# Kernel tuning notes

Measured on AMD Instinct MI355X. Metric: run time of the kernel, lower is better.

## Reference

```python
import jax, jax.numpy as jnp
import numpy as np

H, F, E_SHARED, E_ROUTED, K = 1024, 4096, 1, 8, 2


def setup_inputs() -> dict:
    key = jax.random.key(0)
    ks = jax.random.split(key, 6)
    x = jax.random.normal(ks[0], (4, 2048, H), dtype=jnp.float32)
    s = 0.02
    shared_up = jax.random.normal(ks[1], (E_SHARED, H, F), dtype=jnp.float32) * s
    shared_down = jax.random.normal(ks[2], (E_SHARED, F, H), dtype=jnp.float32) * s
    routed_up = jax.random.normal(ks[3], (E_ROUTED, H, F), dtype=jnp.float32) * s
    routed_down = jax.random.normal(ks[4], (E_ROUTED, F, H), dtype=jnp.float32) * s
    router_w = jax.random.normal(ks[5], (H, E_ROUTED), dtype=jnp.float32) * s
    return {"x": x, "shared_up": shared_up, "shared_down": shared_down,
            "routed_up": routed_up, "routed_down": routed_down, "router_w": router_w}


def _expert(x, w_up, w_down):
    # ExpertBlock: down(gelu(up(x))), exact (erf) gelu as in torch F.gelu default
    h = jax.nn.gelu(jnp.einsum('bsh,hf->bsf', x, w_up), approximate=False)
    return jnp.einsum('bsf,fh->bsh', h, w_down)


def reference(x, shared_up, shared_down, routed_up, routed_down, router_w):
    # shared experts (always active)
    shared_out = jnp.zeros_like(x)
    for i in range(E_SHARED):
        shared_out = shared_out + _expert(x, shared_up[i], shared_down[i])

    # router: softmax over routed experts, then top-k gating
    probs = jax.nn.softmax(jnp.einsum('bsh,he->bse', x, router_w), axis=-1)
    top_k_prob, top_k_idx = jax.lax.top_k(probs, K)  # [B,S,K]
    # per-expert gate = sum of top-k probs assigned to that expert
    onehot = jax.nn.one_hot(top_k_idx, E_ROUTED, dtype=x.dtype)  # [B,S,K,E]
    gates = jnp.einsum('bsk,bske->bse', top_k_prob, onehot)      # [B,S,E]

    routed_out = jnp.zeros_like(x)
    for e in range(E_ROUTED):  # fixed small loop over experts
        y = _expert(x, routed_up[e], routed_down[e])
        routed_out = routed_out + gates[..., e:e + 1] * y

    return shared_out + routed_out + x
```

## Files before the change

### kernel.cpp

```cpp
#include <hip/hip_runtime.h>
#include <cstdint>
#include <cstddef>

#define HD 1024
#define FF 4096
#define TOK 8192
#define NSEG 9
#define ROWS_ROUTED (TOK*2)
#define ROWS_TOT (ROWS_ROUTED + TOK)

typedef __bf16 bf16;
typedef __bf16 bf16x8 __attribute__((ext_vector_type(8)));
typedef __bf16 bf16x4 __attribute__((ext_vector_type(4)));
typedef float  f32x4  __attribute__((ext_vector_type(4)));

__device__ __forceinline__ void stage16(const void* g, void* l) {
  __builtin_amdgcn_global_load_lds((const __attribute__((address_space(1))) void*)g,
                                   (__attribute__((address_space(3))) void*)l,
                                   16, 0, 0);
}

__device__ __forceinline__ unsigned short bf_bits(float v) {
  bf16 b = (bf16)v;
  return __builtin_bit_cast(unsigned short, b);
}

__device__ __forceinline__ int xcd_remap(int d) {
  return (((d >> 6) << 3) + (d & 7)) * 8 + ((d >> 3) & 7);
}

__global__ void k_init_meta(int* meta) {
  int t = threadIdx.x;
  if (t < 64) meta[t] = 0;
}

__global__ void k_tcvt(const float* __restrict__ routed_up, const float* __restrict__ shared_up,
                       const float* __restrict__ routed_dn, const float* __restrict__ shared_dn,
                       bf16* __restrict__ wupT, bf16* __restrict__ wdnT) {
  int z = blockIdx.z;
  bool isup = z < 9;
  int e = isup ? z : z - 9;
  const float* src = isup ? ((e < 8) ? (routed_up + (size_t)e*HD*FF) : shared_up)
                          : ((e < 8) ? (routed_dn + (size_t)e*FF*HD) : shared_dn);
  bf16* d = (isup ? wupT : wdnT) + (size_t)e*FF*HD;
  int R = isup ? HD : FF, C = isup ? FF : HD;
  int r0 = (isup ? blockIdx.y : blockIdx.x) * 64;
  int c0 = (isup ? blockIdx.x : blockIdx.y) * 64;
  __shared__ float lds[64][65];
  int t = threadIdx.x;
  int tr = t>>4, tc4 = (t&15)*4;
  #pragma unroll
  for (int i=0;i<4;i++) {
    float4 v = *reinterpret_cast<const float4*>(src + (size_t)(r0+tr+i*16)*C + c0 + tc4);
    lds[tr+i*16][tc4+0]=v.x; lds[tr+i*16][tc4+1]=v.y;
    lds[tr+i*16][tc4+2]=v.z; lds[tr+i*16][tc4+3]=v.w;
  }
  __syncthreads();
  #pragma unroll
  for (int i=0;i<4;i++) {
    int oc = tr + i*16;
    ushort4 u;
    u.x = bf_bits(lds[tc4+0][oc]);
    u.y = bf_bits(lds[tc4+1][oc]);
    u.z = bf_bits(lds[tc4+2][oc]);
    u.w = bf_bits(lds[tc4+3][oc]);
    *reinterpret_cast<ushort4*>(d + (size_t)(c0+oc)*R + r0 + tc4) = u;
  }
}

__global__ void k_router(const float* __restrict__ x, const float* __restrict__ rw,
                         bf16* __restrict__ xbf,
                         int* __restrict__ rtE, float* __restrict__ rtG,
                         int* __restrict__ meta) {
  __shared__ float rwl[HD*8];
  int t = threadIdx.x;
  for (int i=t;i<HD*8/4;i+=256)
    reinterpret_cast<float4*>(rwl)[i] = reinterpret_cast<const float4*>(rw)[i];
  __syncthreads();
  int wv = t>>6, lane = t&63;
  int tk = blockIdx.x*4 + wv;
  const float* xr = x + (size_t)tk*HD;
  bf16* xb = xbf + (size_t)tk*HD;
  float a[8] = {0,0,0,0,0,0,0,0};
  for (int i=0;i<HD/64;i++) {
    int h = lane + i*64;
    float xv = xr[h];
    xb[h] = (bf16)xv;
    const float* r = rwl + h*8;
    #pragma unroll
    for (int e=0;e<8;e++) a[e] = fmaf(xv, r[e], a[e]);
  }
  #pragma unroll
  for (int e=0;e<8;e++) {
    for (int s=32;s>0;s>>=1) a[e] += __shfl_xor(a[e], s, 64);
  }
  if (lane==0) {
    float mx = a[0];
    #pragma unroll
    for (int e=1;e<8;e++) mx = fmaxf(mx, a[e]);
    float p[8]; float den = 0.f;
    #pragma unroll
    for (int e=0;e<8;e++) { p[e] = expf(a[e]-mx); den += p[e]; }
    int i0 = 0;
    #pragma unroll
    for (int e=1;e<8;e++) if (p[e] > p[i0]) i0 = e;
    int i1 = (i0==0)?1:0;
    #pragma unroll
    for (int e=0;e<8;e++) if (e!=i0 && p[e] > p[i1]) i1 = e;
    float inv = 1.f/den;
    rtE[tk*2] = i0; rtE[tk*2+1] = i1;
    rtG[tk*2] = p[i0]*inv; rtG[tk*2+1] = p[i1]*inv;
    atomicAdd(&meta[i0], 1);
    atomicAdd(&meta[i1], 1);
  }
}

__global__ void k_prefix(int* meta) {
  if (threadIdx.x == 0) {
    int off = 0;
    for (int e=0;e<8;e++) { meta[16+e] = off; meta[32+e] = meta[e]; off += meta[e]; }
    meta[16+8] = ROWS_ROUTED;
    meta[32+8] = TOK;
  }
}

__global__ void k_scatter(const int* __restrict__ rtE, const float* __restrict__ rtG,
                          int* __restrict__ meta, int* __restrict__ tok,
                          float* __restrict__ gate, int* __restrict__ trow) {
  int t = blockIdx.x*256 + threadIdx.x;
  int e0 = rtE[t*2], e1 = rtE[t*2+1];
  float g0 = rtG[t*2], g1 = rtG[t*2+1];
  int p0 = atomicAdd(&meta[8+e0], 1);
  int r0 = meta[16+e0] + p0;
  tok[r0] = t; gate[r0] = g0; trow[t*2] = r0;
  int p1 = atomicAdd(&meta[8+e1], 1);
  int r1 = meta[16+e1] + p1;
  tok[r1] = t; gate[r1] = g1; trow[t*2+1] = r1;
  tok[ROWS_ROUTED + t] = t; gate[ROWS_ROUTED + t] = 1.0f;
}

__global__ void k_combine(const float* __restrict__ x, const bf16* __restrict__ dbuf,
                          const int* __restrict__ trow, float* __restrict__ out) {
  int tkn = blockIdx.x;
  int t = threadIdx.x;
  int r0 = trow[tkn*2], r1 = trow[tkn*2+1];
  int h = t*4;
  float4 xv = *reinterpret_cast<const float4*>(x + (size_t)tkn*HD + h);
  bf16x4 a = *reinterpret_cast<const bf16x4*>(dbuf + (size_t)(ROWS_ROUTED+tkn)*HD + h);
  bf16x4 b = *reinterpret_cast<const bf16x4*>(dbuf + (size_t)r0*HD + h);
  bf16x4 c = *reinterpret_cast<const bf16x4*>(dbuf + (size_t)r1*HD + h);
  float4 o;
  o.x = xv.x + (float)a[0] + (float)b[0] + (float)c[0];
  o.y = xv.y + (float)a[1] + (float)b[1] + (float)c[1];
  o.z = xv.z + (float)a[2] + (float)b[2] + (float)c[2];
  o.w = xv.w + (float)a[3] + (float)b[3] + (float)c[3];
  *reinterpret_cast<float4*>(out + (size_t)tkn*HD + h) = o;
}


#define BUFSZ 24576
#define NKU (HD/32)
#define NKD (FF/32)

__global__ __launch_bounds__(512,4) void k_gemm_up(
    const bf16* __restrict__ xbf, const bf16* __restrict__ wupT,
    bf16* __restrict__ hbuf, const int* __restrict__ tok,
    const int* __restrict__ meta)
{
  int bx = xcd_remap(blockIdx.x);
  int seg = bx >> 10;
  int rem = bx & 1023;
  int mt = rem >> 5, nt = rem & 31;
  int rows = (seg<8)? meta[32+seg] : TOK;
  if (mt*256 >= rows) return;
  int segoff = meta[16+seg];
  int rowbase = mt*256;

  __shared__ __align__(16) char lds[3*BUFSZ];

  const int t = threadIdx.x;
  const int lane = t & 63, w = t >> 6;
  const int wm = w >> 1, wn = w & 1;

  int ar = t>>2;
  int kswz = ((t&3) ^ ((t>>3)&3)) * 8;
  int gr0 = rowbase + ar;        if (gr0 >= rows) gr0 = rows-1;
  int gr1 = rowbase + 128 + ar;  if (gr1 >= rows) gr1 = rows-1;
  const bf16* gA0 = xbf + (size_t)tok[segoff+gr0]*HD + kswz;
  const bf16* gA1 = xbf + (size_t)tok[segoff+gr1]*HD + kswz;
  const bf16* wb = wupT + (size_t)seg*FF*HD;
  const bf16* gB = wb + (size_t)(nt*128 + ar)*HD + kswz;
  const int dA0 = t*16, dA1 = 8192 + t*16, dB = 16384 + t*16;

  const int sx = ((lane>>4) ^ (((lane&15)>>1)&3)) * 16;
  const int Afo = (wm*64 + (lane&15))*64 + sx;
  const int Bfo = 16384 + (wn*64 + (lane&15))*64 + sx;

  f32x4 acc[4][4] = {};

  stage16(gA0,    lds + dA0); stage16(gA1,    lds + dA1); stage16(gB,    lds + dB);
  stage16(gA0+32, lds + BUFSZ + dA0); stage16(gA1+32, lds + BUFSZ + dA1);
  stage16(gB+32,  lds + BUFSZ + dB);
  asm volatile("s_waitcnt vmcnt(3)" ::: "memory");
  __builtin_amdgcn_s_barrier();

  int cur = 0;
  for (int kt = 0; kt < NKU; ++kt) {
    if (kt + 2 < NKU) {
      int st = (cur >= 1) ? cur - 1 : 2;
      int ko = (kt+2)*32;
      char* nb = lds + st*BUFSZ;
      stage16(gA0+ko, nb + dA0); stage16(gA1+ko, nb + dA1); stage16(gB+ko, nb + dB);
    }
    const char* cb = lds + cur*BUFSZ;
    bf16x8 af[4], bfr[4];
    #pragma unroll
    for (int m=0;m<4;m++) af[m]  = *reinterpret_cast<const bf16x8*>(cb + Afo + m*1024);
    #pragma unroll
    for (int n=0;n<4;n++) bfr[n] = *reinterpret_cast<const bf16x8*>(cb + Bfo + n*1024);
    #pragma unroll
    for (int m=0;m<4;m++)
      #pragma unroll
      for (int n=0;n<4;n++)
        acc[m][n] = __builtin_amdgcn_mfma_f32_16x16x32_bf16(bfr[n], af[m], acc[m][n], 0,0,0);
    if (kt + 2 < NKU)      asm volatile("s_waitcnt vmcnt(3)" ::: "memory");
    else if (kt + 1 < NKU) asm volatile("s_waitcnt vmcnt(0)" ::: "memory");
    if (kt + 1 < NKU) __builtin_amdgcn_s_barrier();
    cur = (cur >= 2) ? 0 : cur + 1;
  }

  const int lrm = lane&15, lq = lane>>4;
  #pragma unroll
  for (int m=0;m<4;m++) {
    int rl = wm*64 + m*16 + lrm;
    int gr = rowbase + rl;
    if (gr >= rows) continue;
    bf16* hrow = hbuf + (size_t)(segoff+gr)*FF + nt*128 + wn*64 + lq*4;
    #pragma unroll
    for (int n=0;n<4;n++) {
      bf16x4 u;
      #pragma unroll
      for (int j=0;j<4;j++) {
        float v = acc[m][n][j];
        v = 0.5f*v*(1.0f + erff(v*0.70710678118654752f));
        u[j] = (bf16)v;
      }
      *reinterpret_cast<bf16x4*>(hrow + n*16) = u;
    }
  }
}

__global__ __launch_bounds__(512,4) void k_gemm_down(
    const bf16* __restrict__ hbuf, const bf16* __restrict__ wdnT,
    bf16* __restrict__ dbuf, const float* __restrict__ gate,
    const int* __restrict__ meta)
{
  int bx = xcd_remap(blockIdx.x);
  int seg = bx >> 8;
  int rem = bx & 255;
  int mt = rem >> 3, nt = rem & 7;
  int rows = (seg<8)? meta[32+seg] : TOK;
  if (mt*256 >= rows) return;
  int segoff = meta[16+seg];
  int rowbase = mt*256;

  __shared__ __align__(16) char lds[3*BUFSZ];
  __shared__ float gateL[256];

  const int t = threadIdx.x;
  const int lane = t & 63, w = t >> 6;
  const int wm = w >> 1, wn = w & 1;

  if (t < 256) {
    int gr = rowbase + t; if (gr >= rows) gr = rows - 1;
    gateL[t] = gate[segoff + gr];
  }

  int ar = t>>2;
  int kswz = ((t&3) ^ ((t>>3)&3)) * 8;
  const bf16* gA0 = hbuf + (size_t)(segoff + rowbase + ar)*FF + kswz;
  const bf16* gA1 = hbuf + (size_t)(segoff + rowbase + 128 + ar)*FF + kswz;
  const bf16* wb = wdnT + (size_t)seg*HD*FF;
  const bf16* gB = wb + (size_t)(nt*128 + ar)*FF + kswz;
  const int dA0 = t*16, dA1 = 8192 + t*16, dB = 16384 + t*16;

  const int sx = ((lane>>4) ^ (((lane&15)>>1)&3)) * 16;
  const int Afo = (wm*64 + (lane&15))*64 + sx;
  const int Bfo = 16384 + (wn*64 + (lane&15))*64 + sx;

  f32x4 acc[4][4] = {};

  stage16(gA0,    lds + dA0); stage16(gA1,    lds + dA1); stage16(gB,    lds + dB);
  stage16(gA0+32, lds + BUFSZ + dA0); stage16(gA1+32, lds + BUFSZ + dA1);
  stage16(gB+32,  lds + BUFSZ + dB);
  asm volatile("s_waitcnt vmcnt(3)" ::: "memory");
  __builtin_amdgcn_s_barrier();

  int cur = 0;
  for (int kt = 0; kt < NKD; ++kt) {
    if (kt + 2 < NKD) {
      int st = (cur >= 1) ? cur - 1 : 2;
      int ko = (kt+2)*32;
      char* nb = lds + st*BUFSZ;
      stage16(gA0+ko, nb + dA0); stage16(gA1+ko, nb + dA1); stage16(gB+ko, nb + dB);
    }
    const char* cb = lds + cur*BUFSZ;
    bf16x8 af[4], bfr[4];
    #pragma unroll
    for (int m=0;m<4;m++) af[m]  = *reinterpret_cast<const bf16x8*>(cb + Afo + m*1024);
    #pragma unroll
    for (int n=0;n<4;n++) bfr[n] = *reinterpret_cast<const bf16x8*>(cb + Bfo + n*1024);
    #pragma unroll
    for (int m=0;m<4;m++)
      #pragma unroll
      for (int n=0;n<4;n++)
        acc[m][n] = __builtin_amdgcn_mfma_f32_16x16x32_bf16(bfr[n], af[m], acc[m][n], 0,0,0);
    if (kt + 2 < NKD)      asm volatile("s_waitcnt vmcnt(3)" ::: "memory");
    else if (kt + 1 < NKD) asm volatile("s_waitcnt vmcnt(0)" ::: "memory");
    if (kt + 1 < NKD) __builtin_amdgcn_s_barrier();
    cur = (cur >= 2) ? 0 : cur + 1;
  }

  const int lrm = lane&15, lq = lane>>4;
  #pragma unroll
  for (int m=0;m<4;m++) {
    int rl = wm*64 + m*16 + lrm;
    int gr = rowbase + rl;
    if (gr >= rows) continue;
    float g = gateL[rl];
    bf16* drow = dbuf + (size_t)(segoff+gr)*HD + nt*128 + wn*64 + lq*4;
    #pragma unroll
    for (int n=0;n<4;n++) {
      bf16x4 u;
      #pragma unroll
      for (int j=0;j<4;j++) u[j] = (bf16)(acc[m][n][j]*g);
      *reinterpret_cast<bf16x4*>(drow + n*16) = u;
    }
  }
}

struct Layout {
  size_t xbf, wupT, wdnT, hbuf, dbuf, tok, gate, trow, rtE, rtG, meta, total;
};

static inline Layout make_layout() {
  Layout L; size_t o = 0;
  auto al = [&](size_t b){ o = (o+255)&~(size_t)255; size_t r=o; o+=b; return r; };
  L.xbf  = al((size_t)TOK*HD*2);
  L.wupT = al((size_t)NSEG*FF*HD*2);
  L.wdnT = al((size_t)NSEG*FF*HD*2);
  L.hbuf = al((size_t)ROWS_TOT*FF*2);
  L.dbuf = al((size_t)ROWS_TOT*HD*2);
  L.tok  = al((size_t)ROWS_TOT*4);
  L.gate = al((size_t)ROWS_TOT*4);
  L.trow = al((size_t)TOK*2*4);
  L.rtE  = al((size_t)TOK*2*4);
  L.rtG  = al((size_t)TOK*2*4);
  L.meta = al(256*4);
  L.total = o;
  return L;
}

extern "C" void kernel_launch(void* const* d_in, const int* in_sizes, int n_in,
                              void* d_out, int out_size, void* d_ws, size_t ws_size,
                              hipStream_t stream) {
  const float* x           = (const float*)d_in[0];
  const float* shared_up   = (const float*)d_in[1];
  const float* shared_down = (const float*)d_in[2];
  const float* routed_up   = (const float*)d_in[3];
  const float* routed_down = (const float*)d_in[4];
  const float* router_w    = (const float*)d_in[5];
  float* out = (float*)d_out;

  Layout L = make_layout();
  char* ws = (char*)d_ws;
  bf16*  xbf  = (bf16*)(ws + L.xbf);
  bf16*  wupT = (bf16*)(ws + L.wupT);
  bf16*  wdnT = (bf16*)(ws + L.wdnT);
  bf16*  hbuf = (bf16*)(ws + L.hbuf);
  bf16*  dbuf = (bf16*)(ws + L.dbuf);
  int*   tok  = (int*)(ws + L.tok);
  float* gate = (float*)(ws + L.gate);
  int*   trow = (int*)(ws + L.trow);
  int*   rtE  = (int*)(ws + L.rtE);
  float* rtG  = (float*)(ws + L.rtG);
  int*   meta = (int*)(ws + L.meta);

  k_init_meta<<<1, 64, 0, stream>>>(meta);
  k_tcvt<<<dim3(64, 16, 18), 256, 0, stream>>>(routed_up, shared_up, routed_down, shared_down, wupT, wdnT);
  k_router<<<TOK/4, 256, 0, stream>>>(x, router_w, xbf, rtE, rtG, meta);
  k_prefix<<<1, 64, 0, stream>>>(meta);
  k_scatter<<<TOK/256, 256, 0, stream>>>(rtE, rtG, meta, tok, gate, trow);

  k_gemm_up<<<NSEG*32*32, 512, 0, stream>>>(xbf, wupT, hbuf, tok, meta);
  k_gemm_down<<<NSEG*32*8, 512, 0, stream>>>(hbuf, wdnT, dbuf, gate, meta);
  k_combine<<<TOK, 256, 0, stream>>>(x, dbuf, trow, out);
}
```

Baseline: 988.8 us.

## Fold meta init and prefix into other kernels; double-buffer down GEMM

New measurement: 2.078 ms. +110.2%, slower.

```diff
diff --git a/kernel.cpp b/kernel.cpp
--- a/kernel.cpp
+++ b/kernel.cpp
@@ -29,14 +29,13 @@
   return (((d >> 6) << 3) + (d & 7)) * 8 + ((d >> 3) & 7);
 }
 
-__global__ void k_init_meta(int* meta) {
-  int t = threadIdx.x;
-  if (t < 64) meta[t] = 0;
-}
 
 __global__ void k_tcvt(const float* __restrict__ routed_up, const float* __restrict__ shared_up,
                        const float* __restrict__ routed_dn, const float* __restrict__ shared_dn,
-                       bf16* __restrict__ wupT, bf16* __restrict__ wdnT) {
+                       bf16* __restrict__ wupT, bf16* __restrict__ wdnT,
+                       int* __restrict__ meta) {
+  if (blockIdx.z == 0 && blockIdx.x == 0 && blockIdx.y == 0 && threadIdx.x < 64)
+    meta[threadIdx.x] = 0;
   int z = blockIdx.z;
   bool isup = z < 9;
   int e = isup ? z : z - 9;
@@ -115,28 +114,34 @@
   }
 }
 
-__global__ void k_prefix(int* meta) {
-  if (threadIdx.x == 0) {
-    int off = 0;
-    for (int e=0;e<8;e++) { meta[16+e] = off; meta[32+e] = meta[e]; off += meta[e]; }
-    meta[16+8] = ROWS_ROUTED;
-    meta[32+8] = TOK;
-  }
-}
-
 __global__ void k_scatter(const int* __restrict__ rtE, const float* __restrict__ rtG,
                           int* __restrict__ meta, int* __restrict__ tok,
                           float* __restrict__ gate, int* __restrict__ trow) {
-  int t = blockIdx.x*256 + threadIdx.x;
-  int e0 = rtE[t*2], e1 = rtE[t*2+1];
-  float g0 = rtG[t*2], g1 = rtG[t*2+1];
+  __shared__ int soff[8];
+  int t = threadIdx.x;
+  if (t == 0) {
+    int off = 0;
+    #pragma unroll
+    for (int e=0;e<8;e++) { soff[e] = off; off += meta[e]; }
+    if (blockIdx.x == 0) {
+      int o2 = 0;
+      #pragma unroll
+      for (int e=0;e<8;e++) { meta[16+e] = o2; meta[32+e] = meta[e]; o2 += meta[e]; }
+      meta[16+8] = ROWS_ROUTED;
+      meta[32+8] = TOK;
+    }
+  }
+  __syncthreads();
+  int tk = blockIdx.x*256 + t;
+  int e0 = rtE[tk*2], e1 = rtE[tk*2+1];
+  float g0 = rtG[tk*2], g1 = rtG[tk*2+1];
   int p0 = atomicAdd(&meta[8+e0], 1);
-  int r0 = meta[16+e0] + p0;
-  tok[r0] = t; gate[r0] = g0; trow[t*2] = r0;
+  int r0 = soff[e0] + p0;
+  tok[r0] = tk; gate[r0] = g0; trow[tk*2] = r0;
   int p1 = atomicAdd(&meta[8+e1], 1);
-  int r1 = meta[16+e1] + p1;
-  tok[r1] = t; gate[r1] = g1; trow[t*2+1] = r1;
-  tok[ROWS_ROUTED + t] = t; gate[ROWS_ROUTED + t] = 1.0f;
+  int r1 = soff[e1] + p1;
+  tok[r1] = tk; gate[r1] = g1; trow[tk*2+1] = r1;
+  tok[ROWS_ROUTED + tk] = tk; gate[ROWS_ROUTED + tk] = 1.0f;
 }
 
 __global__ void k_combine(const float* __restrict__ x, const bf16* __restrict__ dbuf,
@@ -250,7 +255,8 @@
   }
 }
 
-__global__ __launch_bounds__(512,4) void k_gemm_down(
+
+__global__ __launch_bounds__(512,6) void k_gemm_down(
     const bf16* __restrict__ hbuf, const bf16* __restrict__ wdnT,
     bf16* __restrict__ dbuf, const float* __restrict__ gate,
     const int* __restrict__ meta)
@@ -264,7 +270,7 @@
   int segoff = meta[16+seg];
   int rowbase = mt*256;
 
-  __shared__ __align__(16) char lds[3*BUFSZ];
+  __shared__ __align__(16) char lds[2*BUFSZ];
   __shared__ float gateL[256];
 
   const int t = threadIdx.x;
@@ -278,8 +284,10 @@
 
   int ar = t>>2;
   int kswz = ((t&3) ^ ((t>>3)&3)) * 8;
-  const bf16* gA0 = hbuf + (size_t)(segoff + rowbase + ar)*FF + kswz;
-  const bf16* gA1 = hbuf + (size_t)(segoff + rowbase + 128 + ar)*FF + kswz;
+  int gr0 = rowbase + ar;        if (gr0 >= rows) gr0 = rows-1;
+  int gr1 = rowbase + 128 + ar;  if (gr1 >= rows) gr1 = rows-1;
+  const bf16* gA0 = hbuf + (size_t)(segoff + gr0)*FF + kswz;
+  const bf16* gA1 = hbuf + (size_t)(segoff + gr1)*FF + kswz;
   const bf16* wb = wdnT + (size_t)seg*HD*FF;
   const bf16* gB = wb + (size_t)(nt*128 + ar)*FF + kswz;
   const int dA0 = t*16, dA1 = 8192 + t*16, dB = 16384 + t*16;
@@ -290,18 +298,14 @@
 
   f32x4 acc[4][4] = {};
 
-  stage16(gA0,    lds + dA0); stage16(gA1,    lds + dA1); stage16(gB,    lds + dB);
-  stage16(gA0+32, lds + BUFSZ + dA0); stage16(gA1+32, lds + BUFSZ + dA1);
-  stage16(gB+32,  lds + BUFSZ + dB);
-  asm volatile("s_waitcnt vmcnt(3)" ::: "memory");
-  __builtin_amdgcn_s_barrier();
+  stage16(gA0, lds + dA0); stage16(gA1, lds + dA1); stage16(gB, lds + dB);
+  __syncthreads();
 
   int cur = 0;
   for (int kt = 0; kt < NKD; ++kt) {
-    if (kt + 2 < NKD) {
-      int st = (cur >= 1) ? cur - 1 : 2;
-      int ko = (kt+2)*32;
-      char* nb = lds + st*BUFSZ;
+    if (kt + 1 < NKD) {
+      int ko = (kt+1)*32;
+      char* nb = lds + (cur^1)*BUFSZ;
       stage16(gA0+ko, nb + dA0); stage16(gA1+ko, nb + dA1); stage16(gB+ko, nb + dB);
     }
     const char* cb = lds + cur*BUFSZ;
@@ -315,10 +319,8 @@
       #pragma unroll
       for (int n=0;n<4;n++)
         acc[m][n] = __builtin_amdgcn_mfma_f32_16x16x32_bf16(bfr[n], af[m], acc[m][n], 0,0,0);
-    if (kt + 2 < NKD)      asm volatile("s_waitcnt vmcnt(3)" ::: "memory");
-    else if (kt + 1 < NKD) asm volatile("s_waitcnt vmcnt(0)" ::: "memory");
-    if (kt + 1 < NKD) __builtin_amdgcn_s_barrier();
-    cur = (cur >= 2) ? 0 : cur + 1;
+    if (kt + 1 < NKD) __syncthreads();
+    cur ^= 1;
   }
 
   const int lrm = lane&15, lq = lane>>4;
@@ -386,10 +388,8 @@
   float* rtG  = (float*)(ws + L.rtG);
   int*   meta = (int*)(ws + L.meta);
 
-  k_init_meta<<<1, 64, 0, stream>>>(meta);
-  k_tcvt<<<dim3(64, 16, 18), 256, 0, stream>>>(routed_up, shared_up, routed_down, shared_down, wupT, wdnT);
+  k_tcvt<<<dim3(64, 16, 18), 256, 0, stream>>>(routed_up, shared_up, routed_down, shared_down, wupT, wdnT, meta);
   k_router<<<TOK/4, 256, 0, stream>>>(x, router_w, xbf, rtE, rtG, meta);
-  k_prefix<<<1, 64, 0, stream>>>(meta);
   k_scatter<<<TOK/256, 256, 0, stream>>>(rtE, rtG, meta, tok, gate, trow);
 
   k_gemm_up<<<NSEG*32*32, 512, 0, stream>>>(xbf, wupT, hbuf, tok, meta);
```
